# Performance work log

Measured on AMD Instinct MI355X. Metric: run time of the kernel, lower is better.

Reference implementation:

```python
import jax, jax.numpy as jnp
import numpy as np

D_MODEL = 1024
N_HEADS = 16
HEAD_DIM = D_MODEL // N_HEADS
EPS = 1e-8  # torch F.cosine_similarity eps


def setup_inputs() -> dict:
    key = jax.random.key(0)
    ks = jax.random.split(key, 5)
    B, S = 2, 2048
    scale = 1.0 / np.sqrt(D_MODEL)
    return {
        "x": jax.random.normal(ks[0], (B, S, D_MODEL), dtype=jnp.float32),
        "W_q": jax.random.normal(ks[1], (D_MODEL, D_MODEL), dtype=jnp.float32) * scale,
        "W_k": jax.random.normal(ks[2], (D_MODEL, D_MODEL), dtype=jnp.float32) * scale,
        "W_v": jax.random.normal(ks[3], (D_MODEL, D_MODEL), dtype=jnp.float32) * scale,
        "W_o": jax.random.normal(ks[4], (D_MODEL, D_MODEL), dtype=jnp.float32) * scale,
    }


def _split_heads(t, B, S):
    # [B,S,D] -> [B,H,S,hd]
    return t.reshape(B, S, N_HEADS, HEAD_DIM).transpose(0, 2, 1, 3)


def reference(x, W_q, W_k, W_v, W_o):
    B, S, _ = x.shape
    Q = _split_heads(x @ W_q.T, B, S)
    K = _split_heads(x @ W_k.T, B, S)
    V = _split_heads(x @ W_v.T, B, S)

    # score[b,h,i,j] = cos_sim(q_i*k_j, ones) = sum_d(q*k) / (||q*k|| * sqrt(hd))
    num = jnp.einsum("bhid,bhjd->bhij", Q, K)
    # ||q_i \odot k_j||^2 = sum_d q^2 k^2, computed as a GEMM (no [B,H,S,S,D] blowup)
    norm_sq = jnp.einsum("bhid,bhjd->bhij", Q * Q, K * K)
    denom = jnp.maximum(jnp.sqrt(norm_sq), EPS) * jnp.sqrt(jnp.float32(HEAD_DIM))
    attn_scores = num / denom

    attn_weights = jax.nn.softmax(attn_scores, axis=-1)
    out = jnp.einsum("bhij,bhjd->bhid", attn_weights, V)
    out = out.transpose(0, 2, 1, 3).reshape(B, S, D_MODEL)
    out = out @ W_o.T
    return out, attn_weights
```

## Files before the change

### kernel.cpp

```cpp
#include <hip/hip_runtime.h>
#include <stdint.h>

typedef __bf16 bf16_t;
typedef __bf16 bf16x4_t __attribute__((ext_vector_type(4)));
typedef __bf16 bf16x8_t __attribute__((ext_vector_type(8)));
typedef float  f32x4_t  __attribute__((ext_vector_type(4)));

#define S_LEN 2048
#define DMODEL 1024
#define NHEAD 16
#define HDIM 64
#define MTOT 4096
#define NT 32
#define WBLK 4864

__device__ __forceinline__ f32x4_t mfma16(bf16x8_t a, bf16x8_t b, f32x4_t c){
  return __builtin_amdgcn_mfma_f32_16x16x32_bf16(a, b, c, 0, 0, 0);
}

__device__ __forceinline__ void gload_lds16(const bf16_t* g, bf16_t* l){
  __builtin_amdgcn_global_load_lds(
      (const __attribute__((address_space(1))) void*)(uintptr_t)g,
      (__attribute__((address_space(3))) void*)(uintptr_t)l,
      16, 0, 0);
}

template<int ROWS>
__device__ __forceinline__ void stage_tile(bf16_t* lds, const bf16_t* __restrict__ g,
                                           int ldg, int wid, int lane){
  const int rl = lane >> 3;
  const int cs = ((lane & 7) ^ rl) << 3;
#pragma unroll
  for (int it = 0; it < ROWS/32; ++it){
    const int chunk = it*4 + wid;
    gload_lds16(g + (size_t)(chunk*8 + rl)*ldg + cs, lds + chunk*512);
  }
}

__device__ __forceinline__ void stage_slice16(bf16_t* lds, const bf16_t* __restrict__ g,
                                              int lane){
  const int rl = lane >> 3;
  const int cs = ((lane & 7) ^ rl) << 3;
#pragma unroll
  for (int c = 0; c < 2; ++c)
    gload_lds16(g + (size_t)(c*8 + rl)*HDIM + cs, lds + c*512);
}

__device__ __forceinline__ void stage_v(bf16_t* lds, const bf16_t* __restrict__ g,
                                        int lane){
#pragma unroll
  for (int c = 0; c < 2; ++c)
    gload_lds16(g + (size_t)lane*64 + c*8, lds + c*512);
}

__device__ __forceinline__ bf16x8_t lds_read8(const bf16_t* t, int row, int ko){
  return *(const bf16x8_t*)&t[row*64 + (ko ^ ((row & 7) << 3))];
}

__device__ __forceinline__ bf16x8_t sq8(bf16x8_t v){
  bf16x8_t r;
#pragma unroll
  for (int i=0;i<8;i++){ float f = (float)v[i]; r[i] = (bf16_t)(f*f); }
  return r;
}

__global__ __launch_bounds__(256)
void vsa_cast_kernel(const float* __restrict__ src, bf16_t* __restrict__ dst, int n4){
  int i = blockIdx.x*256 + threadIdx.x;
  if (i >= n4) return;
  float4 v = ((const float4*)src)[i];
  bf16x4_t o = {(bf16_t)v.x,(bf16_t)v.y,(bf16_t)v.z,(bf16_t)v.w};
  ((bf16x4_t*)dst)[i] = o;
}

__global__ __launch_bounds__(256)
void vsa_qkv_kernel(const bf16_t* __restrict__ xb, const bf16_t* __restrict__ Wb,
                    bf16_t* __restrict__ Qb, bf16_t* __restrict__ Kb,
                    bf16_t* __restrict__ Vblk)
{
  __shared__ __align__(16) bf16_t Ah[128][64], Bh[128][64];
  const int z  = blockIdx.z;
  const int m0 = blockIdx.x * 128;
  const int n0 = blockIdx.y * 128;
  const int tid = threadIdx.x, lane = tid & 63, wid = tid >> 6;
  const int wr = (wid >> 1) * 64, wc = (wid & 1) * 64;
  const bf16_t* Wz = Wb + (size_t)z * (DMODEL*DMODEL);

  const f32x4_t zz = {0.f,0.f,0.f,0.f};
  f32x4_t acc[4][4];
#pragma unroll
  for (int i=0;i<4;i++)
#pragma unroll
    for (int j=0;j<4;j++) acc[i][j] = zz;

  for (int kt = 0; kt < 16; ++kt){
    const int k0 = kt * 64;
    stage_tile<128>(&Ah[0][0], xb + (size_t)m0*DMODEL + k0, DMODEL, wid, lane);
    stage_tile<128>(&Bh[0][0], Wz + (size_t)n0*DMODEL + k0, DMODEL, wid, lane);
    __syncthreads();
#pragma unroll
    for (int kk = 0; kk < 2; ++kk){
      const int ko = kk*32 + (lane>>4)*8;
      bf16x8_t ah[4], bh4[4];
#pragma unroll
      for (int i=0;i<4;i++){
        ah[i]  = lds_read8(&Ah[0][0], wr + i*16 + (lane&15), ko);
        bh4[i] = lds_read8(&Bh[0][0], wc + i*16 + (lane&15), ko);
      }
#pragma unroll
      for (int i=0;i<4;i++)
#pragma unroll
        for (int j=0;j<4;j++)
          acc[i][j] = mfma16(ah[i], bh4[j], acc[i][j]);
    }
    __syncthreads();
  }

#pragma unroll
  for (int i=0;i<4;i++)
#pragma unroll
    for (int j=0;j<4;j++)
#pragma unroll
      for (int r=0;r<4;r++){
        const int m = m0 + wr + i*16 + ((lane>>4)<<2) + r;
        const int n = n0 + wc + j*16 + (lane&15);
        const float q = acc[i][j][r];
        const int b = m >> 11, s = m & 2047, h = n >> 6, d = n & 63;
        const size_t bh_ = (size_t)b*NHEAD + h;
        if (z == 0){
          Qb[(bh_*S_LEN + s)*HDIM + d] = (bf16_t)q;
        } else if (z == 1){
          Kb[(bh_*S_LEN + s)*HDIM + d] = (bf16_t)q;
        } else {
          Vblk[bh_*(size_t)(S_LEN*HDIM) + (size_t)(s>>6)*4096 + d*64 + (s&63)] = (bf16_t)q;
        }
      }
}

__global__ __launch_bounds__(256, 4)
void vsa_attn_kernel(const bf16_t* __restrict__ Qb,
                     const bf16_t* __restrict__ Kb,
                     const bf16_t* __restrict__ Vblk,
                     float* __restrict__ Wout,
                     bf16_t* __restrict__ o1)
{
  __shared__ __align__(16) bf16_t smem[4*WBLK];
  __shared__ float lred[4][2][16];

  const int lin = blockIdx.x;
  const int xcd = lin & 7;
  const int idx = lin >> 3;
  const int qt  = idx & 63;
  const int bh  = xcd + 8*(idx >> 6);
  const int lane = threadIdx.x & 63, w = (int)(threadIdx.x >> 6);
  const int qr = lane & 15, cg = lane >> 4;

  const size_t base = (size_t)bh * (S_LEN*HDIM);
  const bf16_t* Kg = Kb   + base + (size_t)(w*16)*HDIM;
  const bf16_t* Vg = Vblk + base + w*16;

  bf16_t* Kbuf = smem + w*WBLK;
  bf16_t* Vbuf = Kbuf + 2048;
  bf16_t* Pbuf = Vbuf + 2048;

  bf16x8_t aq[2][2], aq2[2][2];
#pragma unroll
  for (int qh = 0; qh < 2; ++qh){
    const bf16_t* qrow = Qb + base + (size_t)(qt*32 + qh*16 + qr)*HDIM;
#pragma unroll
    for (int kk = 0; kk < 2; ++kk){
      aq[qh][kk] = *(const bf16x8_t*)(qrow + kk*32 + cg*8);
      bf16x8_t t;
#pragma unroll
      for (int e=0;e<8;e++){ float f = (float)aq[qh][kk][e]; t[e] = (bf16_t)(64.f*f*f); }
      aq2[qh][kk] = t;
    }
  }

  float lp[2][4] = {{0.f,0.f,0.f,0.f},{0.f,0.f,0.f,0.f}};
  stage_slice16(Kbuf, Kg, lane);
  for (int jt = 0; jt < NT; ++jt){
    const int nb = (jt+1) & (NT-1);
    __builtin_amdgcn_sched_barrier(0);
    stage_slice16(Kbuf + ((jt+1)&1)*1024, Kg + (size_t)nb*64*HDIM, lane);
    asm volatile("s_waitcnt vmcnt(2)" ::: "memory");
    __builtin_amdgcn_sched_barrier(0);
    const bf16_t* kb = Kbuf + (jt&1)*1024;
    bf16x8_t kf0  = lds_read8(kb, qr, cg*8), kf1 = lds_read8(kb, qr, 32+cg*8);
    bf16x8_t k2f0 = sq8(kf0),                k2f1 = sq8(kf1);
    f32x4_t nu[2], nr[2];
    __builtin_amdgcn_s_setprio(1);
#pragma unroll
    for (int qh = 0; qh < 2; ++qh){
      f32x4_t a = {0.f,0.f,0.f,0.f}, b = {0.f,0.f,0.f,0.f};
      a = mfma16(aq[qh][0],  kf0,  a); a = mfma16(aq[qh][1],  kf1,  a);
      b = mfma16(aq2[qh][0], k2f0, b); b = mfma16(aq2[qh][1], k2f1, b);
      nu[qh] = a; nr[qh] = b;
    }
    __builtin_amdgcn_s_setprio(0);
#pragma unroll
    for (int qh = 0; qh < 2; ++qh)
#pragma unroll
      for (int r=0;r<4;r++){
        const float s = nu[qh][r]*rsqrtf(fmaxf(nr[qh][r], 6.4e-15f));
        lp[qh][r] += __expf(s);
      }
  }

#pragma unroll
  for (int qh=0;qh<2;qh++)
#pragma unroll
    for (int r=0;r<4;r++){
      float l = lp[qh][r];
      l += __shfl_xor(l,1); l += __shfl_xor(l,2);
      l += __shfl_xor(l,4); l += __shfl_xor(l,8);
      lred[w][qh][cg*4+r] = l;
    }
  __syncthreads();
  float rl[2][4];
#pragma unroll
  for (int qh=0;qh<2;qh++)
#pragma unroll
    for (int r=0;r<4;r++)
      rl[qh][r] = 1.0f/(lred[0][qh][cg*4+r]+lred[1][qh][cg*4+r]
                       +lred[2][qh][cg*4+r]+lred[3][qh][cg*4+r]);

  const f32x4_t zz = {0.f,0.f,0.f,0.f};
  f32x4_t oacc[2][4];
#pragma unroll
  for (int qh=0;qh<2;qh++)
#pragma unroll
    for (int n=0;n<4;n++) oacc[qh][n] = zz;
  const size_t wb = (size_t)bh * S_LEN * S_LEN;
  const bf16x8_t zero8 = {};

  stage_v(Vbuf, Vg, lane);
  asm volatile("s_waitcnt vmcnt(0)" ::: "memory");
  __builtin_amdgcn_sched_barrier(0);

  for (int jt = 0; jt < NT; ++jt){
    const int nb = (jt+1) & (NT-1);
    __builtin_amdgcn_sched_barrier(0);
    stage_slice16(Kbuf + ((jt+1)&1)*1024, Kg + (size_t)nb*64*HDIM, lane);
    stage_v(Vbuf + ((jt+1)&1)*1024, Vg + (size_t)nb*4096, lane);
    asm volatile("s_waitcnt vmcnt(12)" ::: "memory");
    __builtin_amdgcn_sched_barrier(0);
    const bf16_t* kb = Kbuf + (jt&1)*1024;
    bf16x8_t kf0  = lds_read8(kb, qr, cg*8), kf1 = lds_read8(kb, qr, 32+cg*8);
    bf16x8_t k2f0 = sq8(kf0),                k2f1 = sq8(kf1);
    f32x4_t nu[2], nr[2];
    __builtin_amdgcn_s_setprio(1);
#pragma unroll
    for (int qh = 0; qh < 2; ++qh){
      f32x4_t a = {0.f,0.f,0.f,0.f}, b = {0.f,0.f,0.f,0.f};
      a = mfma16(aq[qh][0],  kf0,  a); a = mfma16(aq[qh][1],  kf1,  a);
      b = mfma16(aq2[qh][0], k2f0, b); b = mfma16(aq2[qh][1], k2f1, b);
      nu[qh] = a; nr[qh] = b;
    }
    __builtin_amdgcn_s_setprio(0);
#pragma unroll
    for (int qh = 0; qh < 2; ++qh)
#pragma unroll
      for (int r=0;r<4;r++){
        const float s = nu[qh][r]*rsqrtf(fmaxf(nr[qh][r], 6.4e-15f));
        const float wgt = __expf(s) * rl[qh][r];
        const int i = qt*32 + qh*16 + cg*4 + r;
        const int j = jt*64 + w*16 + qr;
        Wout[wb + (size_t)i*S_LEN + j] = wgt;
        Pbuf[qh*384 + (cg*4+r)*24 + qr] = (bf16_t)wgt;
      }
    asm volatile("s_waitcnt lgkmcnt(0)" ::: "memory");
    __builtin_amdgcn_sched_barrier(0);
    const int k0 = (cg & 1) * 8;
    bf16x8_t pa0 = (cg < 2) ? *(const bf16x8_t*)&Pbuf[      qr*24 + k0] : zero8;
    bf16x8_t pa1 = (cg < 2) ? *(const bf16x8_t*)&Pbuf[384 + qr*24 + k0] : zero8;
    const bf16_t* vbase = Vbuf + (jt&1)*1024 + (cg&1)*512;
    __builtin_amdgcn_s_setprio(1);
#pragma unroll
    for (int n=0;n<4;n++){
      bf16x8_t vb = *(const bf16x8_t*)&vbase[(n*16+qr)*8];
      oacc[0][n] = mfma16(pa0, vb, oacc[0][n]);
      oacc[1][n] = mfma16(pa1, vb, oacc[1][n]);
    }
    __builtin_amdgcn_s_setprio(0);
  }

  asm volatile("s_waitcnt vmcnt(0)" ::: "memory");
  __builtin_amdgcn_sched_barrier(0);
  float* Ow = (float*)Kbuf;
#pragma unroll
  for (int qh=0;qh<2;qh++)
#pragma unroll
    for (int n=0;n<4;n++)
#pragma unroll
      for (int r=0;r<4;r++)
        Ow[(qh*16+cg*4+r)*68 + n*16+qr] = oacc[qh][n][r];
  __syncthreads();
  {
    const int row = lane >> 1;
    const int jl  = (lane & 1)*8;
    float v[8];
#pragma unroll
    for (int e=0;e<8;e++) v[e] = 0.f;
#pragma unroll
    for (int ww=0; ww<4; ++ww){
      const float* Os = (const float*)(smem + ww*WBLK);
#pragma unroll
      for (int e=0;e<8;e++) v[e] += Os[row*68 + w*16 + jl + e];
    }
    const int b = bh >> 4, h = bh & 15;
    const int srow = qt*32 + row;
    const size_t o = ((size_t)b*S_LEN + srow)*DMODEL + (size_t)h*HDIM + w*16 + jl;
    bf16x8_t hv;
#pragma unroll
    for (int e=0;e<8;e++) hv[e] = (bf16_t)v[e];
    *(bf16x8_t*)(o1 + o) = hv;
  }
}

__global__ __launch_bounds__(256)
void vsa_oproj_kernel(const bf16_t* __restrict__ Ab, const bf16_t* __restrict__ Bb,
                      float* __restrict__ out)
{
  __shared__ __align__(16) bf16_t Ah[64][64], Bh[128][64];
  const int m0 = blockIdx.x * 64;
  const int n0 = blockIdx.y * 128;
  const int tid = threadIdx.x, lane = tid & 63, wid = tid >> 6;
  const int wc = wid * 32;

  const f32x4_t zz = {0.f,0.f,0.f,0.f};
  f32x4_t acc[4][2];
#pragma unroll
  for (int i=0;i<4;i++)
#pragma unroll
    for (int j=0;j<2;j++) acc[i][j] = zz;

  for (int kt = 0; kt < 16; ++kt){
    const int k0 = kt * 64;
    stage_tile<64> (&Ah[0][0], Ab + (size_t)m0*DMODEL + k0, DMODEL, wid, lane);
    stage_tile<128>(&Bh[0][0], Bb + (size_t)n0*DMODEL + k0, DMODEL, wid, lane);
    __syncthreads();
#pragma unroll
    for (int kk = 0; kk < 2; ++kk){
      const int ko = kk*32 + (lane>>4)*8;
      bf16x8_t ah[4], bh4[2];
#pragma unroll
      for (int i=0;i<4;i++)
        ah[i] = lds_read8(&Ah[0][0], i*16 + (lane&15), ko);
#pragma unroll
      for (int j=0;j<2;j++)
        bh4[j] = lds_read8(&Bh[0][0], wc + j*16 + (lane&15), ko);
#pragma unroll
      for (int i=0;i<4;i++)
#pragma unroll
        for (int j=0;j<2;j++)
          acc[i][j] = mfma16(ah[i], bh4[j], acc[i][j]);
    }
    __syncthreads();
  }

#pragma unroll
  for (int i=0;i<4;i++)
#pragma unroll
    for (int j=0;j<2;j++)
#pragma unroll
      for (int r=0;r<4;r++){
        const int m = m0 + i*16 + ((lane>>4)<<2) + r;
        const int n = n0 + wc + j*16 + (lane&15);
        out[(size_t)m*DMODEL + n] = acc[i][j][r];
      }
}

extern "C" void kernel_launch(void* const* d_in, const int* in_sizes, int n_in,
                              void* d_out, int out_size, void* d_ws, size_t ws_size,
                              hipStream_t stream)
{
  const float* x  = (const float*)d_in[0];
  const float* Wq = (const float*)d_in[1];
  const float* Wk = (const float*)d_in[2];
  const float* Wv = (const float*)d_in[3];
  const float* Wo = (const float*)d_in[4];
  float* out  = (float*)d_out;
  float* attw = out + (size_t)MTOT*DMODEL;

  bf16_t* ws = (bf16_t*)d_ws;
  const size_t C = 4194304;
  bf16_t* xb   = ws;
  bf16_t* Wb   = ws + C;
  bf16_t* Qb   = ws + 2*C;
  bf16_t* Kb   = ws + 3*C;
  bf16_t* Vblk = ws + 4*C;
  bf16_t* o1   = ws + 5*C;

  const int W1 = DMODEL*DMODEL;
  vsa_cast_kernel<<<(int)(C/1024), 256, 0, stream>>>(x,  xb, (int)(C/4));
  vsa_cast_kernel<<<W1/1024, 256, 0, stream>>>(Wq, Wb + 0*(size_t)W1, W1/4);
  vsa_cast_kernel<<<W1/1024, 256, 0, stream>>>(Wk, Wb + 1*(size_t)W1, W1/4);
  vsa_cast_kernel<<<W1/1024, 256, 0, stream>>>(Wv, Wb + 2*(size_t)W1, W1/4);
  vsa_cast_kernel<<<W1/1024, 256, 0, stream>>>(Wo, Wb + 3*(size_t)W1, W1/4);

  vsa_qkv_kernel<<<dim3(32, 8, 3), 256, 0, stream>>>(xb, Wb, Qb, Kb, Vblk);
  vsa_attn_kernel<<<dim3(2048), 256, 0, stream>>>(Qb, Kb, Vblk, attw, o1);
  vsa_oproj_kernel<<<dim3(64, 8), 256, 0, stream>>>(o1, Wb + 3*(size_t)W1, out);
}
```

Measured before the change: 308.7 us.

## Split softmax row-sum pass into separate kernel with direct global K loads

Moves the first pass, which computes the softmax denominators, out of the attention kernel into a new lsum kernel. In that kernel each wave owns 16 query rows and walks all keys itself using register-prefetched global loads instead of LDS staging. The attention kernel then reads the precomputed row sums from a workspace buffer and skips its own first K sweep and the block-level reduction sync. This removes the in-block cross-wave reduction and LDS traffic in pass one, at the cost of an extra kernel launch, an extra global buffer, and uncoalesced K reads from global memory.

```diff
diff --git a/kernel.cpp b/kernel.cpp
--- a/kernel.cpp
+++ b/kernel.cpp
@@ -137,15 +137,80 @@
       }
 }
 
+__global__ __launch_bounds__(256)
+void vsa_lsum_kernel(const bf16_t* __restrict__ Qb, const bf16_t* __restrict__ Kb,
+                     float* __restrict__ lbuf)
+{
+  const int lin = blockIdx.x;
+  const int xcd = lin & 7;
+  const int idx = lin >> 3;
+  const int qb  = idx & 31;
+  const int bh  = xcd + 8*(idx >> 5);
+  const int lane = threadIdx.x & 63, w = (int)(threadIdx.x >> 6);
+  const int qr = lane & 15, cg = lane >> 4;
+
+  const size_t base = (size_t)bh * (S_LEN*HDIM);
+
+  bf16x8_t aq[2], aq2[2];
+  {
+    const bf16_t* qrow = Qb + base + (size_t)(qb*64 + w*16 + qr)*HDIM;
+#pragma unroll
+    for (int kk = 0; kk < 2; ++kk){
+      aq[kk] = *(const bf16x8_t*)(qrow + kk*32 + cg*8);
+      bf16x8_t t;
+#pragma unroll
+      for (int e=0;e<8;e++){ float f = (float)aq[kk][e]; t[e] = (bf16_t)(64.f*f*f); }
+      aq2[kk] = t;
+    }
+  }
+
+  const bf16_t* krow = Kb + base + (size_t)qr*HDIM + cg*8;
+
+  float lp[4] = {0.f,0.f,0.f,0.f};
+  bf16x8_t nf0 = *(const bf16x8_t*)(krow);
+  bf16x8_t nf1 = *(const bf16x8_t*)(krow + 32);
+  for (int jf = 0; jf < 128; ++jf){
+    bf16x8_t kf0 = nf0, kf1 = nf1;
+    const int nj = (jf+1) & 127;
+    const bf16_t* nx = krow + (size_t)nj*(16*HDIM);
+    nf0 = *(const bf16x8_t*)(nx);
+    nf1 = *(const bf16x8_t*)(nx + 32);
+    f32x4_t nu = {0.f,0.f,0.f,0.f}, nr_ = {0.f,0.f,0.f,0.f};
+    nu  = mfma16(aq[0],  kf0,      nu );
+    nu  = mfma16(aq[1],  kf1,      nu );
+    nr_ = mfma16(aq2[0], sq8(kf0), nr_);
+    nr_ = mfma16(aq2[1], sq8(kf1), nr_);
+#pragma unroll
+    for (int r=0;r<4;r++){
+      const float s = nu[r]*rsqrtf(fmaxf(nr_[r], 6.4e-15f));
+      lp[r] += __expf(s);
+    }
+  }
+
+  float lr[4];
+#pragma unroll
+  for (int r=0;r<4;r++){
+    float l = lp[r];
+    l += __shfl_xor(l,1); l += __shfl_xor(l,2);
+    l += __shfl_xor(l,4); l += __shfl_xor(l,8);
+    lr[r] = l;
+  }
+  if (qr == 0){
+    float* dst = lbuf + bh*S_LEN + qb*64 + w*16 + cg*4;
+#pragma unroll
+    for (int r=0;r<4;r++) dst[r] = lr[r];
+  }
+}
+
 __global__ __launch_bounds__(256, 4)
 void vsa_attn_kernel(const bf16_t* __restrict__ Qb,
                      const bf16_t* __restrict__ Kb,
                      const bf16_t* __restrict__ Vblk,
+                     const float* __restrict__ lbuf,
                      float* __restrict__ Wout,
                      bf16_t* __restrict__ o1)
 {
   __shared__ __align__(16) bf16_t smem[4*WBLK];
-  __shared__ float lred[4][2][16];
 
   const int lin = blockIdx.x;
   const int xcd = lin & 7;
@@ -177,53 +242,12 @@
     }
   }
 
-  float lp[2][4] = {{0.f,0.f,0.f,0.f},{0.f,0.f,0.f,0.f}};
-  stage_slice16(Kbuf, Kg, lane);
-  for (int jt = 0; jt < NT; ++jt){
-    const int nb = (jt+1) & (NT-1);
-    __builtin_amdgcn_sched_barrier(0);
-    stage_slice16(Kbuf + ((jt+1)&1)*1024, Kg + (size_t)nb*64*HDIM, lane);
-    asm volatile("s_waitcnt vmcnt(2)" ::: "memory");
-    __builtin_amdgcn_sched_barrier(0);
-    const bf16_t* kb = Kbuf + (jt&1)*1024;
-    bf16x8_t kf0  = lds_read8(kb, qr, cg*8), kf1 = lds_read8(kb, qr, 32+cg*8);
-    bf16x8_t k2f0 = sq8(kf0),                k2f1 = sq8(kf1);
-    f32x4_t nu[2], nr[2];
-    __builtin_amdgcn_s_setprio(1);
-#pragma unroll
-    for (int qh = 0; qh < 2; ++qh){
-      f32x4_t a = {0.f,0.f,0.f,0.f}, b = {0.f,0.f,0.f,0.f};
-      a = mfma16(aq[qh][0],  kf0,  a); a = mfma16(aq[qh][1],  kf1,  a);
-      b = mfma16(aq2[qh][0], k2f0, b); b = mfma16(aq2[qh][1], k2f1, b);
-      nu[qh] = a; nr[qh] = b;
-    }
-    __builtin_amdgcn_s_setprio(0);
-#pragma unroll
-    for (int qh = 0; qh < 2; ++qh)
-#pragma unroll
-      for (int r=0;r<4;r++){
-        const float s = nu[qh][r]*rsqrtf(fmaxf(nr[qh][r], 6.4e-15f));
-        lp[qh][r] += __expf(s);
-      }
-  }
-
+  float rl[2][4];
 #pragma unroll
   for (int qh=0;qh<2;qh++)
 #pragma unroll
-    for (int r=0;r<4;r++){
-      float l = lp[qh][r];
-      l += __shfl_xor(l,1); l += __shfl_xor(l,2);
-      l += __shfl_xor(l,4); l += __shfl_xor(l,8);
-      lred[w][qh][cg*4+r] = l;
-    }
-  __syncthreads();
-  float rl[2][4];
-#pragma unroll
-  for (int qh=0;qh<2;qh++)
-#pragma unroll
     for (int r=0;r<4;r++)
-      rl[qh][r] = 1.0f/(lred[0][qh][cg*4+r]+lred[1][qh][cg*4+r]
-                       +lred[2][qh][cg*4+r]+lred[3][qh][cg*4+r]);
+      rl[qh][r] = 1.0f / lbuf[bh*S_LEN + qt*32 + qh*16 + cg*4 + r];
 
   const f32x4_t zz = {0.f,0.f,0.f,0.f};
   f32x4_t oacc[2][4];
@@ -234,6 +258,7 @@
   const size_t wb = (size_t)bh * S_LEN * S_LEN;
   const bf16x8_t zero8 = {};
 
+  stage_slice16(Kbuf, Kg, lane);
   stage_v(Vbuf, Vg, lane);
   asm volatile("s_waitcnt vmcnt(0)" ::: "memory");
   __builtin_amdgcn_sched_barrier(0);
@@ -391,6 +416,7 @@
   bf16_t* Kb   = ws + 3*C;
   bf16_t* Vblk = ws + 4*C;
   bf16_t* o1   = ws + 5*C;
+  float*  lbuf = (float*)(ws + 6*C);
 
   const int W1 = DMODEL*DMODEL;
   vsa_cast_kernel<<<(int)(C/1024), 256, 0, stream>>>(x,  xb, (int)(C/4));
@@ -400,6 +426,7 @@
   vsa_cast_kernel<<<W1/1024, 256, 0, stream>>>(Wo, Wb + 3*(size_t)W1, W1/4);
 
   vsa_qkv_kernel<<<dim3(32, 8, 3), 256, 0, stream>>>(xb, Wb, Qb, Kb, Vblk);
-  vsa_attn_kernel<<<dim3(2048), 256, 0, stream>>>(Qb, Kb, Vblk, attw, o1);
+  vsa_lsum_kernel<<<dim3(1024), 256, 0, stream>>>(Qb, Kb, lbuf);
+  vsa_attn_kernel<<<dim3(2048), 256, 0, stream>>>(Qb, Kb, Vblk, lbuf, attw, o1);
   vsa_oproj_kernel<<<dim3(64, 8), 256, 0, stream>>>(o1, Wb + 3*(size_t)W1, out);
 }
```

Measured after the change: 419.9 us. +36.0%, slower.
